# Kernel tuning notes

Measured on AMD Instinct MI355X. Metric: run time of the kernel, lower is better.

## Reference

```python
import jax, jax.numpy as jnp
import numpy as np

MARGIN = 0.3
N_CLASSES = 1024
N_SAMPLES = 32
D = 512


def setup_inputs() -> dict:
    key = jax.random.key(0)
    k1, k2 = jax.random.split(key)
    embeddings = jax.random.normal(k1, (2 * N_CLASSES * N_SAMPLES, D), dtype=jnp.float32)
    target = jax.random.randint(k2, (2 * N_CLASSES * N_SAMPLES,), 0, N_CLASSES, dtype=jnp.int64)
    return {"embeddings": embeddings, "target": target}


def reference(embeddings, target):
    # [C, 2, S, D]: per class, block 0 = positives, block 1 = negatives
    e = embeddings.reshape(N_CLASSES, 2, N_SAMPLES, D)
    pos = e[:, 0]  # [C, S, D]
    neg = e[:, 1]  # [C, S, D]
    anchor = pos.mean(axis=1, keepdims=True)  # [C, 1, D]
    ap = jnp.sum((anchor - pos) ** 2, axis=-1)  # [C, S]
    neg_d = jnp.sum((neg - anchor) ** 2, axis=-1)  # [C, S]
    # an_distances = dist(anchor, nearest negative) == min over negatives
    an = jnp.min(neg_d, axis=1, keepdims=True)  # [C, 1]
    losses = jnp.sum(jax.nn.relu(ap - an + MARGIN), axis=1)  # [C]
    return losses.mean()
```

## Files before the change

### kernel.cpp

```cpp
#include <hip/hip_runtime.h>

#define NC 1024
#define NS 32
#define DD 512
#define MARGIN 0.3f

__global__ __launch_bounds__(256) void ccl_per_class(const float* __restrict__ emb,
                                                     float* __restrict__ class_loss) {
    const int c = blockIdx.x;
    const int t = threadIdx.x;
    const float* pos = emb + (size_t)c * (2 * NS * DD);
    const float* neg = pos + NS * DD;

    __shared__ float s_anchor[DD];
    __shared__ float s_ap[NS];
    __shared__ float s_nd[NS];

    const int col4 = t & 127;
    const int g = t >> 7;
    const float4* posv = (const float4*)pos;
    float4 acc = make_float4(0.f, 0.f, 0.f, 0.f);
#pragma unroll
    for (int s = 0; s < NS / 2; ++s) {
        float4 v = posv[(2 * s + g) * (DD / 4) + col4];
        acc.x += v.x; acc.y += v.y; acc.z += v.z; acc.w += v.w;
    }
    if (g == 0) {
        ((float4*)s_anchor)[col4] = acc;
    }
    __syncthreads();
    if (g == 1) {
        float4 o = ((float4*)s_anchor)[col4];
        o.x = (o.x + acc.x) * (1.f / NS);
        o.y = (o.y + acc.y) * (1.f / NS);
        o.z = (o.z + acc.z) * (1.f / NS);
        o.w = (o.w + acc.w) * (1.f / NS);
        ((float4*)s_anchor)[col4] = o;
    }
    __syncthreads();

    const int s = t >> 3;
    const int k = t & 7;
    const float4* negv = (const float4*)neg;
    const float4* anch = (const float4*)s_anchor;
    float ap = 0.f, nd = 0.f;
#pragma unroll
    for (int i = 0; i < DD / 4 / 8; ++i) {
        const int c4 = k + 8 * i;
        const float4 a = anch[c4];
        float4 p = posv[s * (DD / 4) + c4];
        float dx = p.x - a.x, dy = p.y - a.y, dz = p.z - a.z, dw = p.w - a.w;
        ap += dx * dx + dy * dy + dz * dz + dw * dw;
        float4 n = negv[s * (DD / 4) + c4];
        dx = n.x - a.x; dy = n.y - a.y; dz = n.z - a.z; dw = n.w - a.w;
        nd += dx * dx + dy * dy + dz * dz + dw * dw;
    }
#pragma unroll
    for (int m = 1; m < 8; m <<= 1) {
        ap += __shfl_xor(ap, m);
        nd += __shfl_xor(nd, m);
    }
    if (k == 0) { s_ap[s] = ap; s_nd[s] = nd; }
    __syncthreads();

    if (t == 0) {
        float an = s_nd[0];
#pragma unroll
        for (int j = 1; j < NS; ++j) an = fminf(an, s_nd[j]);
        float loss = 0.f;
#pragma unroll
        for (int j = 0; j < NS; ++j) loss += fmaxf(s_ap[j] - an + MARGIN, 0.f);
        class_loss[c] = loss;
    }
}

__global__ __launch_bounds__(256) void ccl_reduce(const float* __restrict__ class_loss,
                                                  float* __restrict__ out) {
    const int t = threadIdx.x;
    float v = class_loss[t] + class_loss[t + 256] + class_loss[t + 512] + class_loss[t + 768];
#pragma unroll
    for (int m = 32; m >= 1; m >>= 1) v += __shfl_down(v, m);
    __shared__ float s_partial[4];
    if ((t & 63) == 0) s_partial[t >> 6] = v;
    __syncthreads();
    if (t == 0)
        out[0] = (s_partial[0] + s_partial[1] + s_partial[2] + s_partial[3]) * (1.f / NC);
}

extern "C" void kernel_launch(void* const* d_in, const int* in_sizes, int n_in,
                              void* d_out, int out_size, void* d_ws, size_t ws_size,
                              hipStream_t stream) {
    const float* emb = (const float*)d_in[0];
    float* cls = (float*)d_ws;
    float* out = (float*)d_out;
    ccl_per_class<<<NC, 256, 0, stream>>>(emb, cls);
    ccl_reduce<<<1, 256, 0, stream>>>(cls, out);
}
```

Baseline: 33.16 us.

## Load class rows once into registers and reuse for anchor and distances

Each thread now loads its 16 positive and 16 negative float4 rows into registers up front. It uses them both to build the anchor mean and to compute the squared distances, so the second global pass over the positives and the negatives is gone. Per-row distances are reduced with full-wavefront xor shuffles of 32 values, and the final min/sum runs with warp shuffles instead of a serial thread-0 loop. This raises register pressure to about 128 VGPRs for the data plus the shuffle work, which may reduce occupancy.

```diff
diff --git a/kernel.cpp b/kernel.cpp
--- a/kernel.cpp
+++ b/kernel.cpp
@@ -9,68 +9,76 @@
                                                      float* __restrict__ class_loss) {
     const int c = blockIdx.x;
     const int t = threadIdx.x;
-    const float* pos = emb + (size_t)c * (2 * NS * DD);
-    const float* neg = pos + NS * DD;
+    const int g = t >> 7;
+    const int col4 = t & 127;
+    const float4* posv = (const float4*)(emb + (size_t)c * (2 * NS * DD));
+    const float4* negv = posv + NS * DD / 4;
 
-    __shared__ float s_anchor[DD];
-    __shared__ float s_ap[NS];
-    __shared__ float s_nd[NS];
+    __shared__ float4 s_part[2][128];
+    __shared__ float4 s_anchor[128];
+    __shared__ float s_wap[4][16];
+    __shared__ float s_wnd[4][16];
 
-    const int col4 = t & 127;
-    const int g = t >> 7;
-    const float4* posv = (const float4*)pos;
-    float4 acc = make_float4(0.f, 0.f, 0.f, 0.f);
+    float4 p[16], n[16];
 #pragma unroll
-    for (int s = 0; s < NS / 2; ++s) {
-        float4 v = posv[(2 * s + g) * (DD / 4) + col4];
-        acc.x += v.x; acc.y += v.y; acc.z += v.z; acc.w += v.w;
+    for (int j = 0; j < 16; ++j) p[j] = posv[(2 * j + g) * (DD / 4) + col4];
+#pragma unroll
+    for (int j = 0; j < 16; ++j) n[j] = negv[(2 * j + g) * (DD / 4) + col4];
+
+    float4 acc = p[0];
+#pragma unroll
+    for (int j = 1; j < 16; ++j) {
+        acc.x += p[j].x; acc.y += p[j].y; acc.z += p[j].z; acc.w += p[j].w;
     }
-    if (g == 0) {
-        ((float4*)s_anchor)[col4] = acc;
-    }
+    s_part[g][col4] = acc;
     __syncthreads();
-    if (g == 1) {
-        float4 o = ((float4*)s_anchor)[col4];
-        o.x = (o.x + acc.x) * (1.f / NS);
-        o.y = (o.y + acc.y) * (1.f / NS);
-        o.z = (o.z + acc.z) * (1.f / NS);
-        o.w = (o.w + acc.w) * (1.f / NS);
-        ((float4*)s_anchor)[col4] = o;
+    if (t < 128) {
+        float4 a = s_part[0][t];
+        float4 b = s_part[1][t];
+        a.x = (a.x + b.x) * (1.f / NS);
+        a.y = (a.y + b.y) * (1.f / NS);
+        a.z = (a.z + b.z) * (1.f / NS);
+        a.w = (a.w + b.w) * (1.f / NS);
+        s_anchor[t] = a;
     }
     __syncthreads();
 
-    const int s = t >> 3;
-    const int k = t & 7;
-    const float4* negv = (const float4*)neg;
-    const float4* anch = (const float4*)s_anchor;
-    float ap = 0.f, nd = 0.f;
+    const float4 a = s_anchor[col4];
+    float apc[16], ndc[16];
 #pragma unroll
-    for (int i = 0; i < DD / 4 / 8; ++i) {
-        const int c4 = k + 8 * i;
-        const float4 a = anch[c4];
-        float4 p = posv[s * (DD / 4) + c4];
-        float dx = p.x - a.x, dy = p.y - a.y, dz = p.z - a.z, dw = p.w - a.w;
-        ap += dx * dx + dy * dy + dz * dz + dw * dw;
-        float4 n = negv[s * (DD / 4) + c4];
-        dx = n.x - a.x; dy = n.y - a.y; dz = n.z - a.z; dw = n.w - a.w;
-        nd += dx * dx + dy * dy + dz * dz + dw * dw;
+    for (int j = 0; j < 16; ++j) {
+        float dx = p[j].x - a.x, dy = p[j].y - a.y, dz = p[j].z - a.z, dw = p[j].w - a.w;
+        apc[j] = dx * dx + dy * dy + dz * dz + dw * dw;
+        dx = n[j].x - a.x; dy = n[j].y - a.y; dz = n[j].z - a.z; dw = n[j].w - a.w;
+        ndc[j] = dx * dx + dy * dy + dz * dz + dw * dw;
     }
+
 #pragma unroll
-    for (int m = 1; m < 8; m <<= 1) {
-        ap += __shfl_xor(ap, m);
-        nd += __shfl_xor(nd, m);
+    for (int m = 1; m < 64; m <<= 1) {
+#pragma unroll
+        for (int j = 0; j < 16; ++j) {
+            apc[j] += __shfl_xor(apc[j], m);
+            ndc[j] += __shfl_xor(ndc[j], m);
+        }
     }
-    if (k == 0) { s_ap[s] = ap; s_nd[s] = nd; }
+    const int wv = t >> 6;
+    if ((t & 63) == 0) {
+#pragma unroll
+        for (int j = 0; j < 16; ++j) { s_wap[wv][j] = apc[j]; s_wnd[wv][j] = ndc[j]; }
+    }
     __syncthreads();
 
-    if (t == 0) {
-        float an = s_nd[0];
+    if (t < NS) {
+        const int sg = t & 1, sj = t >> 1;
+        float ap = s_wap[2 * sg][sj] + s_wap[2 * sg + 1][sj];
+        float nd = s_wnd[2 * sg][sj] + s_wnd[2 * sg + 1][sj];
+        float an = nd;
 #pragma unroll
-        for (int j = 1; j < NS; ++j) an = fminf(an, s_nd[j]);
-        float loss = 0.f;
+        for (int m = 1; m < 32; m <<= 1) an = fminf(an, __shfl_xor(an, m));
+        float l = fmaxf(ap - an + MARGIN, 0.f);
 #pragma unroll
-        for (int j = 0; j < NS; ++j) loss += fmaxf(s_ap[j] - an + MARGIN, 0.f);
-        class_loss[c] = loss;
+        for (int m = 1; m < 32; m <<= 1) l += __shfl_xor(l, m);
+        if (t == 0) class_loss[c] = l;
     }
 }
 
```

Result: faster. 29.61 us (-10.7%).
